# Performance work log

Measured on AMD Instinct MI355X. Metric: run time of the kernel, lower is better.

## Reference

```python
import jax, jax.numpy as jnp
import numpy as np

B, S, V, E, H, L = 16, 256, 32000, 512, 1024, 2


def setup_inputs() -> dict:
    key = jax.random.key(0)
    ks = jax.random.split(key, 10)
    scale = 0.02
    tokens = jax.random.randint(ks[0], (B, S), 1, V)  # avoid pad token 0
    emb = jax.random.normal(ks[1], (V, E), dtype=jnp.float32) * scale
    W0 = jax.random.normal(ks[2], (E, 4 * H), dtype=jnp.float32) * scale
    U0 = jax.random.normal(ks[3], (H, 4 * H), dtype=jnp.float32) * scale
    b0 = jnp.zeros((4 * H,), dtype=jnp.float32)
    W1 = jax.random.normal(ks[4], (H, 4 * H), dtype=jnp.float32) * scale
    U1 = jax.random.normal(ks[5], (H, 4 * H), dtype=jnp.float32) * scale
    b1 = jnp.zeros((4 * H,), dtype=jnp.float32)
    Wd = jax.random.normal(ks[6], (H, V), dtype=jnp.float32) * scale
    bd = jnp.zeros((V,), dtype=jnp.float32)
    return {"tokens": tokens, "emb": emb, "W0": W0, "U0": U0, "b0": b0,
            "W1": W1, "U1": U1, "b1": b1, "Wd": Wd, "bd": bd}


def lstm_layer(x, mask, W, U, b):
    """Keras LSTM (gate order i,f,g,o), mask carries state/output on padded steps.
    x: [B,S,D], mask: [B,S] bool -> (ys [B,S,H], h [B,H], c [B,H])."""
    h_dim = U.shape[0]
    bsz = x.shape[0]
    x_t = jnp.swapaxes(x, 0, 1)           # [S,B,D]
    m_t = jnp.swapaxes(mask, 0, 1)        # [S,B]

    def step(carry, inp):
        h, c = carry
        xt, mt = inp
        z = xt @ W + h @ U + b            # [B,4H]
        i, f, g, o = jnp.split(z, 4, axis=-1)
        c_new = jax.nn.sigmoid(f) * c + jax.nn.sigmoid(i) * jnp.tanh(g)
        h_new = jax.nn.sigmoid(o) * jnp.tanh(c_new)
        mt = mt[:, None]
        h_new = jnp.where(mt, h_new, h)
        c_new = jnp.where(mt, c_new, c)
        return (h_new, c_new), h_new

    init = (jnp.zeros((bsz, h_dim), x.dtype), jnp.zeros((bsz, h_dim), x.dtype))
    (h, c), ys = jax.lax.scan(step, init, (x_t, m_t))
    return jnp.swapaxes(ys, 0, 1), h, c


def reference(tokens, emb, W0, U0, b0, W1, U1, b1, Wd, bd):
    mask = tokens != 0                    # mask_zero=True in Embedding
    x = emb[tokens]                       # [B,S,E]
    x, h0, c0 = lstm_layer(x, mask, W0, U0, b0)
    x, h1, c1 = lstm_layer(x, mask, W1, U1, b1)
    probs = jax.nn.softmax(x @ Wd + bd, axis=-1)  # Dense(softmax) -> [B,S,V]
    h_stack = jnp.stack([h0, h1])         # [L,B,H] final hidden states
    c_stack = jnp.stack([c0, c1])         # [L,B,H] final cell states
    return probs, h_stack, c_stack
```

## Files before the change

kernel.cpp:

```cpp
#include <hip/hip_runtime.h>

typedef __attribute__((ext_vector_type(8))) short bf16x8;
typedef __attribute__((ext_vector_type(4))) float f32x4;

#define S_LEN 256
#define VOCAB 32000
#define EMB   512
#define HID   1024

static const size_t OUT_H = 131072000ull;

__device__ inline unsigned short f2bf(float f) {
  unsigned int u = __float_as_uint(f);
  u = (u + 0x7FFFu + ((u >> 16) & 1u)) >> 16;
  return (unsigned short)u;
}
__device__ inline float bf2f(unsigned short s) {
  return __uint_as_float(((unsigned int)s) << 16);
}

__device__ inline void st_h(unsigned short* p, unsigned short v) {
  __hip_atomic_store(p, v, __ATOMIC_RELAXED, __HIP_MEMORY_SCOPE_AGENT);
}

__device__ inline int xcd_swz(int o, int n) {
  int q = n >> 3, r = n & 7;
  int x = o & 7, i = o >> 3;
  return (x < r ? x * (q + 1) : r * (q + 1) + (x - r) * q) + i;
}

__device__ inline void gload16(const void* g, void* lds) {
  __builtin_amdgcn_global_load_lds((const __attribute__((address_space(1))) unsigned int*)g,
                                   (__attribute__((address_space(3))) unsigned int*)lds,
                                   16, 0, 0);
}

__global__ __launch_bounds__(256) void k_transpose_bf16(const float* __restrict__ src,
                                                        unsigned short* __restrict__ dst,
                                                        int K, int N) {
  __shared__ float tile[64][65];
  int n0 = blockIdx.x * 64, k0 = blockIdx.y * 64;
  int tid = threadIdx.x;
#pragma unroll
  for (int i = 0; i < 16; ++i) {
    int e = tid + i * 256;
    int r = e >> 6, c = e & 63;
    tile[r][c] = src[(size_t)(k0 + r) * N + n0 + c];
  }
  __syncthreads();
#pragma unroll
  for (int i = 0; i < 16; ++i) {
    int e = tid + i * 256;
    int r = e >> 6, c = e & 63;
    dst[(size_t)(n0 + r) * K + k0 + c] = f2bf(tile[c][r]);
  }
}

__global__ __launch_bounds__(256) void k_gather_emb(const int* __restrict__ tokens,
                                                    const float* __restrict__ emb,
                                                    unsigned short* __restrict__ Xg) {
  int r = blockIdx.x;
  int s = r >> 4, b = r & 15;
  int tok = tokens[b * S_LEN + s];
  const float* src = emb + (size_t)tok * EMB;
  int k = threadIdx.x * 2;
  float2 v = *(const float2*)(src + k);
  ushort2 o; o.x = f2bf(v.x); o.y = f2bf(v.y);
  *(ushort2*)(Xg + (size_t)r * EMB + k) = o;
}

__global__ __launch_bounds__(256) void k_gemm128(const unsigned short* __restrict__ A,
                                                 const unsigned short* __restrict__ BT,
                                                 float* __restrict__ C,
                                                 const float* __restrict__ bias,
                                                 int M, int N, int K) {
  __shared__ unsigned short As[4096];
  __shared__ unsigned short Bs[4096];
  int tid = threadIdx.x;
  int lane = tid & 63, wv = tid >> 6;
  int wr = wv >> 1, wc = wv & 1;
  int bxs = xcd_swz(blockIdx.x, gridDim.x);
  int am0 = blockIdx.y * 128, bn0 = bxs * 128;
  f32x4 zero = {0.f, 0.f, 0.f, 0.f};
  f32x4 acc[4][4];
#pragma unroll
  for (int m = 0; m < 4; ++m)
#pragma unroll
    for (int n = 0; n < 4; ++n) acc[m][n] = zero;
  int KT = K >> 5;
  int lr = lane & 15, kq = lane >> 4;
  for (int kt = 0; kt < KT; ++kt) {
    int k0 = kt << 5;
    __syncthreads();
#pragma unroll
    for (int c = 0; c < 2; ++c) {
      int t2 = c * 256 + tid;
      int row = t2 & 127, kg = t2 >> 7;
      gload16(A + (size_t)(am0 + row) * K + k0 + kg * 8, &As[(c * 256 + wv * 64) * 8]);
    }
#pragma unroll
    for (int c = 0; c < 2; ++c) {
      int t2 = c * 256 + tid;
      int row = t2 & 127, kg = t2 >> 7;
      gload16(BT + (size_t)(bn0 + row) * K + k0 + kg * 8, &Bs[(c * 256 + wv * 64) * 8]);
    }
    __syncthreads();
    const bf16x8* Ap = (const bf16x8*)As;
    const bf16x8* Bp = (const bf16x8*)Bs;
    bf16x8 af[4], bf[4];
#pragma unroll
    for (int m = 0; m < 4; ++m) af[m] = Ap[kq * 128 + wr * 64 + m * 16 + lr];
#pragma unroll
    for (int n = 0; n < 4; ++n) bf[n] = Bp[kq * 128 + wc * 64 + n * 16 + lr];
#pragma unroll
    for (int m = 0; m < 4; ++m)
#pragma unroll
      for (int n = 0; n < 4; ++n)
        acc[m][n] = __builtin_amdgcn_mfma_f32_16x16x32_bf16(af[m], bf[n], acc[m][n], 0, 0, 0);
  }
#pragma unroll
  for (int m = 0; m < 4; ++m)
#pragma unroll
    for (int n = 0; n < 4; ++n) {
      int col = bn0 + wc * 64 + n * 16 + lr;
      float bv = bias ? bias[col] : 0.f;
#pragma unroll
      for (int q = 0; q < 4; ++q) {
        int row = am0 + wr * 64 + m * 16 + kq * 4 + q;
        C[(size_t)row * N + col] = acc[m][n][q] + bv;
      }
    }
}

__global__ __launch_bounds__(512, 2) void k_gemm256(const unsigned short* __restrict__ A,
                                                    const unsigned short* __restrict__ BT,
                                                    unsigned short* __restrict__ Cb,
                                                    const float* __restrict__ bias,
                                                    int M, int N, int K,
                                                    float* __restrict__ Mpart,
                                                    float* __restrict__ Spart,
                                                    int NT) {
  extern __shared__ unsigned short lds[];
  int tid = threadIdx.x;
  int w = tid >> 6, lane = tid & 63;
  int wr = w >> 2, wcn = w & 3;
  int lr = lane & 15, kq = lane >> 4, sw = lr & 7;
  int bxs = xcd_swz(blockIdx.x, gridDim.x);
  int gm0 = blockIdx.y * 256, gn0 = bxs * 256;
  const int KT = K >> 6;

  f32x4 acc[8][4];
#pragma unroll
  for (int m = 0; m < 8; ++m)
#pragma unroll
    for (int n = 0; n < 4; ++n) acc[m][n] = f32x4{0.f, 0.f, 0.f, 0.f};

  auto stage = [&](const unsigned short* g, int grow0, int kt, int mat, int half) {
    unsigned short* sb = lds + ((((kt & 1) * 2 + mat) * 2 + half) << 13);
#pragma unroll
    for (int ld = 0; ld < 2; ++ld) {
      int j = ld * 512 + tid;
      int row = j >> 3, c16 = j & 7;
      const unsigned short* src =
          g + (size_t)(grow0 + half * 128 + row) * K + kt * 64 + ((c16 ^ (row & 7)) << 3);
      gload16(src, sb + ((ld * 512 + w * 64) << 3));
    }
  };

  stage(A, gm0, 0, 0, 0); stage(A, gm0, 0, 0, 1);
  stage(BT, gn0, 0, 1, 0); stage(BT, gn0, 0, 1, 1);
  stage(BT, gn0, 1, 1, 0); stage(BT, gn0, 1, 1, 1);
  asm volatile("s_waitcnt vmcnt(4)" ::: "memory");
  __builtin_amdgcn_sched_barrier(0);
  __builtin_amdgcn_s_barrier();

  const int halfB = wcn >> 1;
  const int rowB0 = (wcn & 1) * 64;

  for (int i = 0; i < KT / 2; ++i) {
    int kt0 = 2 * i, kt1 = 2 * i + 1;
#pragma unroll
    for (int half = 0; half < 2; ++half) {
      int kt = half ? kt1 : kt0;
      int buf = kt & 1;
      const unsigned short* ldsA = lds + (((buf * 2 + 0) * 2 + wr) << 13);
      const unsigned short* ldsB = lds + (((buf * 2 + 1) * 2 + halfB) << 13);
      bf16x8 bf[4][2];
#pragma unroll
      for (int qd = 0; qd < 4; ++qd) {
        if (qd == 0) {
#pragma unroll
          for (int fn = 0; fn < 4; ++fn)
#pragma unroll
            for (int kk = 0; kk < 2; ++kk) {
              int r = rowB0 + fn * 16 + lr;
              int c = (kk * 4 + kq) ^ sw;
              bf[fn][kk] = *(const bf16x8*)(ldsB + r * 64 + c * 8);
            }
        }
        bf16x8 af[2][2];
#pragma unroll
        for (int m2 = 0; m2 < 2; ++m2)
#pragma unroll
          for (int kk = 0; kk < 2; ++kk) {
            int r = (qd * 2 + m2) * 16 + lr;
            int c = (kk * 4 + kq) ^ sw;
            af[m2][kk] = *(const bf16x8*)(ldsA + r * 64 + c * 8);
          }
        if (half == 0) {
          if (qd == 0) { stage(A, gm0, kt0 + 1, 0, 0); stage(A, gm0, kt0 + 1, 0, 1); }
          else if (qd == 1) { if (kt0 + 2 < KT) stage(BT, gn0, kt0 + 2, 1, 0); }
          else if (qd == 2) { if (kt0 + 2 < KT) stage(BT, gn0, kt0 + 2, 1, 1); }
          else {
            if (kt0 + 2 < KT) asm volatile("s_waitcnt vmcnt(4)" ::: "memory");
            else              asm volatile("s_waitcnt vmcnt(0)" ::: "memory");
          }
        } else {
          if (qd == 0)      { if (kt1 + 1 < KT) stage(A, gm0, kt1 + 1, 0, 0); }
          else if (qd == 1) { if (kt1 + 1 < KT) stage(A, gm0, kt1 + 1, 0, 1); }
          else if (qd == 2) { if (kt1 + 2 < KT) stage(BT, gn0, kt1 + 2, 1, 0); }
          else {
            if (kt1 + 2 < KT) { stage(BT, gn0, kt1 + 2, 1, 1);
                                asm volatile("s_waitcnt vmcnt(4)" ::: "memory"); }
            else              asm volatile("s_waitcnt vmcnt(0)" ::: "memory");
          }
        }
        __builtin_amdgcn_sched_barrier(0);
        __builtin_amdgcn_s_barrier();
        asm volatile("s_waitcnt lgkmcnt(0)" ::: "memory");
        __builtin_amdgcn_sched_barrier(0);
        __builtin_amdgcn_s_setprio(1);
#pragma unroll
        for (int m2 = 0; m2 < 2; ++m2)
#pragma unroll
          for (int n = 0; n < 4; ++n)
#pragma unroll
            for (int kk = 0; kk < 2; ++kk)
              acc[qd * 2 + m2][n] =
                  __builtin_amdgcn_mfma_f32_16x16x32_bf16(af[m2][kk], bf[n][kk],
                                                          acc[qd * 2 + m2][n], 0, 0, 0);
        __builtin_amdgcn_s_setprio(0);
        __builtin_amdgcn_sched_barrier(0);
        __builtin_amdgcn_s_barrier();
      }
    }
  }

  asm volatile("s_waitcnt vmcnt(0) lgkmcnt(0)" ::: "memory");
  __syncthreads();

  float bvc[4];
#pragma unroll
  for (int n = 0; n < 4; ++n) bvc[n] = bias[gn0 + wcn * 64 + n * 16 + lr];
#pragma unroll
  for (int fm = 0; fm < 8; ++fm)
#pragma unroll
    for (int n = 0; n < 4; ++n) {
      int col = gn0 + wcn * 64 + n * 16 + lr;
#pragma unroll
      for (int q = 0; q < 4; ++q) {
        int row = gm0 + wr * 128 + fm * 16 + kq * 4 + q;
        Cb[(size_t)row * N + col] = f2bf(acc[fm][n][q] + bvc[n]);
      }
    }
  float* redM = (float*)lds;
  float* redS = (float*)lds + 1024;
#pragma unroll
  for (int fm = 0; fm < 8; ++fm)
#pragma unroll
    for (int q = 0; q < 4; ++q) {
      float mx = fmaxf(fmaxf(acc[fm][0][q] + bvc[0], acc[fm][1][q] + bvc[1]),
                       fmaxf(acc[fm][2][q] + bvc[2], acc[fm][3][q] + bvc[3]));
#pragma unroll
      for (int off = 1; off < 16; off <<= 1) mx = fmaxf(mx, __shfl_xor(mx, off));
      if (lr == 0) redM[(wr * 4 + wcn) * 128 + fm * 16 + kq * 4 + q] = mx;
    }
  __syncthreads();
#pragma unroll
  for (int fm = 0; fm < 8; ++fm)
#pragma unroll
    for (int q = 0; q < 4; ++q) {
      int idx = fm * 16 + kq * 4 + q;
      float mxF = fmaxf(fmaxf(redM[(wr * 4 + 0) * 128 + idx], redM[(wr * 4 + 1) * 128 + idx]),
                        fmaxf(redM[(wr * 4 + 2) * 128 + idx], redM[(wr * 4 + 3) * 128 + idx]));
      float s = __expf(acc[fm][0][q] + bvc[0] - mxF) + __expf(acc[fm][1][q] + bvc[1] - mxF) +
                __expf(acc[fm][2][q] + bvc[2] - mxF) + __expf(acc[fm][3][q] + bvc[3] - mxF);
#pragma unroll
      for (int off = 1; off < 16; off <<= 1) s += __shfl_xor(s, off);
      if (lr == 0) redS[(wr * 4 + wcn) * 128 + idx] = s;
    }
  __syncthreads();
  if (wcn == 0 && lr == 0) {
#pragma unroll
    for (int fm = 0; fm < 8; ++fm)
#pragma unroll
      for (int q = 0; q < 4; ++q) {
        int idx = fm * 16 + kq * 4 + q;
        float mxF = fmaxf(fmaxf(redM[(wr * 4 + 0) * 128 + idx], redM[(wr * 4 + 1) * 128 + idx]),
                          fmaxf(redM[(wr * 4 + 2) * 128 + idx], redM[(wr * 4 + 3) * 128 + idx]));
        float ss = redS[(wr * 4 + 0) * 128 + idx] + redS[(wr * 4 + 1) * 128 + idx] +
                   redS[(wr * 4 + 2) * 128 + idx] + redS[(wr * 4 + 3) * 128 + idx];
        int row = gm0 + wr * 128 + idx;
        Mpart[(size_t)row * NT + bxs] = mxF;
        Spart[(size_t)row * NT + bxs] = ss;
      }
  }
}

__global__ __launch_bounds__(256) void k_sm_combine(const float* __restrict__ Mp,
                                                    const float* __restrict__ Sp,
                                                    float* __restrict__ MS, int T) {
  int row = blockIdx.x * 4 + (threadIdx.x >> 6);
  int lane = threadIdx.x & 63;
  float mx = -3.4e38f;
  for (int i = lane; i < T; i += 64) mx = fmaxf(mx, Mp[(size_t)row * T + i]);
#pragma unroll
  for (int o = 32; o > 0; o >>= 1) mx = fmaxf(mx, __shfl_xor(mx, o));
  float s = 0.f;
  for (int i = lane; i < T; i += 64)
    s += Sp[(size_t)row * T + i] * __expf(Mp[(size_t)row * T + i] - mx);
#pragma unroll
  for (int o = 32; o > 0; o >>= 1) s += __shfl_xor(s, o);
  if (lane == 0) { MS[row * 2] = mx; MS[row * 2 + 1] = 1.f / s; }
}

__global__ __launch_bounds__(256) void k_sm_apply_bf16(const unsigned short* __restrict__ lg,
                                                       float* __restrict__ probs,
                                                       const float* __restrict__ MS) {
  const int total = 4096 * (VOCAB / 4);
  for (int idx = blockIdx.x * 256 + threadIdx.x; idx < total; idx += gridDim.x * 256) {
    int row = idx / (VOCAB / 4);
    float M = MS[row * 2], inv = MS[row * 2 + 1];
    ushort4 v = ((const ushort4*)lg)[idx];
    float4 o;
    o.x = __expf(bf2f(v.x) - M) * inv;
    o.y = __expf(bf2f(v.y) - M) * inv;
    o.z = __expf(bf2f(v.z) - M) * inv;
    o.w = __expf(bf2f(v.w) - M) * inv;
    ((float4*)probs)[idx] = o;
  }
}

struct LstmSmem {
  unsigned short U0s[16384];
  unsigned short W1s[16384];
  unsigned short U1s[16384];
  float zA[4][16][16];
  float zB[4][16][16];
  float c0[16][4], h0f[16][4], c1[16][4], h1f[16][4];
  float b1s[16];
  short toks[16][256];
  unsigned short h0st[16][4], h1st[16][4];
};

__global__ __launch_bounds__(256, 1) void k_lstm(const int* __restrict__ tokens,
                                                 const float* __restrict__ XW,
                                                 const unsigned short* __restrict__ U0T,
                                                 const unsigned short* __restrict__ W1T,
                                                 const unsigned short* __restrict__ U1T,
                                                 const float* __restrict__ b1,
                                                 unsigned short* __restrict__ h0r,
                                                 unsigned short* __restrict__ h1r,
                                                 unsigned short* __restrict__ Y1,
                                                 float* outHC,
                                                 int* bar) {
  extern __shared__ char smraw[];
  LstmSmem& sm = *(LstmSmem*)smraw;
  int tid = threadIdx.x, bid = blockIdx.x;
  int lane = tid & 63, wv = tid >> 6;

  for (int idx = tid; idx < 2048; idx += 256) {
    int cidx = idx >> 7, kg = idx & 127;
    int gcol = (cidx >> 2) * 1024 + bid * 4 + (cidx & 3);
    *(uint4*)&sm.U0s[(kg * 16 + cidx) * 8] = *(const uint4*)&U0T[(size_t)gcol * 1024 + kg * 8];
    *(uint4*)&sm.W1s[(kg * 16 + cidx) * 8] = *(const uint4*)&W1T[(size_t)gcol * 1024 + kg * 8];
    *(uint4*)&sm.U1s[(kg * 16 + cidx) * 8] = *(const uint4*)&U1T[(size_t)gcol * 1024 + kg * 8];
  }
  for (int idx = tid; idx < 4096; idx += 256) {
    sm.toks[idx >> 8][idx & 255] = (short)tokens[idx];
  }
  if (tid < 64) {
    int b = tid >> 2, u = tid & 3;
    sm.c0[b][u] = 0.f; sm.h0f[b][u] = 0.f;
    sm.c1[b][u] = 0.f; sm.h1f[b][u] = 0.f;
  }
  if (tid < 16) sm.b1s[tid] = b1[(tid >> 2) * 1024 + bid * 4 + (tid & 3)];
  __syncthreads();

  int lr = lane & 15, kq = lane >> 4;

  auto gbar = [&](int gen) {
    __syncthreads();
    if (tid == 0)
      __hip_atomic_store(&bar[bid * 16], gen, __ATOMIC_RELAXED, __HIP_MEMORY_SCOPE_AGENT);
    int ok;
    do {
      int f = __hip_atomic_load(&bar[tid * 16], __ATOMIC_RELAXED, __HIP_MEMORY_SCOPE_AGENT);
      ok = (f >= gen);
    } while (!__syncthreads_and(ok));
  };

  if (wv == 1) {
    int l = tid - 64, b = l >> 2, u = l & 3;
    const float* xp = XW + (size_t)b * 4096 + bid * 4 + u;
    float z0 = xp[0], z2 = xp[2048], z3 = xp[3072];
    float ii = 1.f / (1.f + expf(-z0));
    float gg = tanhf(z2);
    float oo = 1.f / (1.f + expf(-z3));
    float cn = ii * gg;
    float hn = oo * tanhf(cn);
    if (sm.toks[b][0] == 0) { cn = 0.f; hn = 0.f; }
    sm.c0[b][u] = cn; sm.h0f[b][u] = hn;
    st_h(h0r + b * HID + bid * 4 + u, f2bf(hn));
  }
  gbar(1);

  for (int t = 0; t < 255; ++t) {
    const unsigned short* h0t = h0r + (size_t)t * 16384;
    const unsigned short* h1p = h1r + (size_t)(t > 0 ? t - 1 : 0) * 16384;
    unsigned short* h1c = h1r + (size_t)t * 16384;
    unsigned short* h0n = h0r + (size_t)(t + 1) * 16384;

    float xwv0 = 0, xwv1 = 0, xwv2 = 0, xwv3 = 0;
    if (wv == 1) {
      int l = tid - 64, b = l >> 2, u = l & 3;
      const float* xp = XW + ((size_t)(t + 1) * 16 + b) * 4096 + bid * 4 + u;
      xwv0 = xp[0]; xwv1 = xp[1024]; xwv2 = xp[2048]; xwv3 = xp[3072];
    }

    f32x4 accB = {0.f, 0.f, 0.f, 0.f};
    {
      const unsigned short* ap = (wv < 2) ? h0t : h1p;
      const unsigned short* bm = (wv < 2) ? sm.W1s : sm.U1s;
      int kofs = (wv & 1) * 512;
      if (wv < 2 || t > 0) {
#pragma unroll
        for (int s8 = 0; s8 < 16; ++s8) {
          int kb = kofs + s8 * 32;
          bf16x8 av = *(const bf16x8*)(ap + lr * HID + kb + kq * 8);
          bf16x8 bv = *(const bf16x8*)&bm[(((kb >> 3) + kq) * 16 + lr) * 8];
          accB = __builtin_amdgcn_mfma_f32_16x16x32_bf16(av, bv, accB, 0, 0, 0);
        }
      }
    }
    f32x4 accA = {0.f, 0.f, 0.f, 0.f};
#pragma unroll
    for (int s8 = 0; s8 < 8; ++s8) {
      int kb = wv * 256 + s8 * 32;
      bf16x8 av = *(const bf16x8*)(h0t + lr * HID + kb + kq * 8);
      bf16x8 bv = *(const bf16x8*)&sm.U0s[(((kb >> 3) + kq) * 16 + lr) * 8];
      accA = __builtin_amdgcn_mfma_f32_16x16x32_bf16(av, bv, accA, 0, 0, 0);
    }
#pragma unroll
    for (int q = 0; q < 4; ++q) {
      sm.zB[wv][kq * 4 + q][lr] = accB[q];
      sm.zA[wv][kq * 4 + q][lr] = accA[q];
    }
    __syncthreads();

    if (wv == 0) {
      int b = tid >> 2, u = tid & 3;
      int tok = sm.toks[b][t];
      float z0 = sm.b1s[0 + u]  + sm.zB[0][b][0 + u]  + sm.zB[1][b][0 + u]  + sm.zB[2][b][0 + u]  + sm.zB[3][b][0 + u];
      float z1 = sm.b1s[4 + u]  + sm.zB[0][b][4 + u]  + sm.zB[1][b][4 + u]  + sm.zB[2][b][4 + u]  + sm.zB[3][b][4 + u];
      float z2 = sm.b1s[8 + u]  + sm.zB[0][b][8 + u]  + sm.zB[1][b][8 + u]  + sm.zB[2][b][8 + u]  + sm.zB[3][b][8 + u];
      float z3 = sm.b1s[12 + u] + sm.zB[0][b][12 + u] + sm.zB[1][b][12 + u] + sm.zB[2][b][12 + u] + sm.zB[3][b][12 + u];
      float ii = 1.f / (1.f + expf(-z0));
      float ff = 1.f / (1.f + expf(-z1));
      float gg = tanhf(z2);
      float oo = 1.f / (1.f + expf(-z3));
      float cold = sm.c1[b][u], hold = sm.h1f[b][u];
      float cn = ff * cold + ii * gg;
      float hn = oo * tanhf(cn);
      if (tok == 0) { cn = cold; hn = hold; }
      sm.c1[b][u] = cn; sm.h1f[b][u] = hn;
      unsigned short hb = f2bf(hn);
      sm.h1st[b][u] = hb;
      Y1[((size_t)b * S_LEN + t) * HID + bid * 4 + u] = hb;
    } else if (wv == 1) {
      int l = tid - 64, b = l >> 2, u = l & 3;
      int tok = sm.toks[b][t + 1];
      float z0 = xwv0 + sm.zA[0][b][0 + u]  + sm.zA[1][b][0 + u]  + sm.zA[2][b][0 + u]  + sm.zA[3][b][0 + u];
      float z1 = xwv1 + sm.zA[0][b][4 + u]  + sm.zA[1][b][4 + u]  + sm.zA[2][b][4 + u]  + sm.zA[3][b][4 + u];
      float z2 = xwv2 + sm.zA[0][b][8 + u]  + sm.zA[1][b][8 + u]  + sm.zA[2][b][8 + u]  + sm.zA[3][b][8 + u];
      float z3 = xwv3 + sm.zA[0][b][12 + u] + sm.zA[1][b][12 + u] + sm.zA[2][b][12 + u] + sm.zA[3][b][12 + u];
      float ii = 1.f / (1.f + expf(-z0));
      float ff = 1.f / (1.f + expf(-z1));
      float gg = tanhf(z2);
      float oo = 1.f / (1.f + expf(-z3));
      float cold = sm.c0[b][u], hold = sm.h0f[b][u];
      float cn = ff * cold + ii * gg;
      float hn = oo * tanhf(cn);
      if (tok == 0) { cn = cold; hn = hold; }
      sm.c0[b][u] = cn; sm.h0f[b][u] = hn;
      sm.h0st[b][u] = f2bf(hn);
    }
    __syncthreads();
    if (tid < 32) {
      int b = tid & 15;
      unsigned long long v = *(const unsigned long long*)((tid < 16) ? &sm.h1st[b][0]
                                                                     : &sm.h0st[b][0]);
      unsigned short* dst = (tid < 16) ? (h1c + b * HID + bid * 4)
                                       : (h0n + b * HID + bid * 4);
      __hip_atomic_store((unsigned long long*)dst, v, __ATOMIC_RELAXED,
                         __HIP_MEMORY_SCOPE_AGENT);
    }
    gbar(t + 2);
  }

  {
    const unsigned short* h0t = h0r + 255ull * 16384;
    const unsigned short* h1p = h1r + 254ull * 16384;
    f32x4 accB = {0.f, 0.f, 0.f, 0.f};
    const unsigned short* ap = (wv < 2) ? h0t : h1p;
    const unsigned short* bm = (wv < 2) ? sm.W1s : sm.U1s;
    int kofs = (wv & 1) * 512;
#pragma unroll
    for (int s8 = 0; s8 < 16; ++s8) {
      int kb = kofs + s8 * 32;
      bf16x8 av = *(const bf16x8*)(ap + lr * HID + kb + kq * 8);
      bf16x8 bv = *(const bf16x8*)&bm[(((kb >> 3) + kq) * 16 + lr) * 8];
      accB = __builtin_amdgcn_mfma_f32_16x16x32_bf16(av, bv, accB, 0, 0, 0);
    }
#pragma unroll
    for (int q = 0; q < 4; ++q) sm.zB[wv][kq * 4 + q][lr] = accB[q];
    __syncthreads();
    if (wv == 0) {
      int b = tid >> 2, u = tid & 3;
      int tok = sm.toks[b][255];
      float z0 = sm.b1s[0 + u]  + sm.zB[0][b][0 + u]  + sm.zB[1][b][0 + u]  + sm.zB[2][b][0 + u]  + sm.zB[3][b][0 + u];
      float z1 = sm.b1s[4 + u]  + sm.zB[0][b][4 + u]  + sm.zB[1][b][4 + u]  + sm.zB[2][b][4 + u]  + sm.zB[3][b][4 + u];
      float z2 = sm.b1s[8 + u]  + sm.zB[0][b][8 + u]  + sm.zB[1][b][8 + u]  + sm.zB[2][b][8 + u]  + sm.zB[3][b][8 + u];
      float z3 = sm.b1s[12 + u] + sm.zB[0][b][12 + u] + sm.zB[1][b][12 + u] + sm.zB[2][b][12 + u] + sm.zB[3][b][12 + u];
      float ii = 1.f / (1.f + expf(-z0));
      float ff = 1.f / (1.f + expf(-z1));
      float gg = tanhf(z2);
      float oo = 1.f / (1.f + expf(-z3));
      float cold = sm.c1[b][u], hold = sm.h1f[b][u];
      float cn = ff * cold + ii * gg;
      float hn = oo * tanhf(cn);
      if (tok == 0) { cn = cold; hn = hold; }
      sm.c1[b][u] = cn; sm.h1f[b][u] = hn;
      Y1[((size_t)b * S_LEN + 255) * HID + bid * 4 + u] = f2bf(hn);
    }
    __syncthreads();
  }

  if (tid < 64) {
    int b = tid >> 2, u = tid & 3, ug = bid * 4 + u;
    outHC[OUT_H + (size_t)b * HID + ug]         = sm.h0f[b][u];
    outHC[OUT_H + 16384 + (size_t)b * HID + ug] = sm.h1f[b][u];
    outHC[OUT_H + 32768 + (size_t)b * HID + ug] = sm.c0[b][u];
    outHC[OUT_H + 49152 + (size_t)b * HID + ug] = sm.c1[b][u];
  }
}

extern "C" void kernel_launch(void* const* d_in, const int* in_sizes, int n_in,
                              void* d_out, int out_size, void* d_ws, size_t ws_size,
                              hipStream_t stream) {
  const int*   tokens = (const int*)d_in[0];
  const float* emb = (const float*)d_in[1];
  const float* W0  = (const float*)d_in[2];
  const float* U0  = (const float*)d_in[3];
  const float* b0  = (const float*)d_in[4];
  const float* W1  = (const float*)d_in[5];
  const float* U1  = (const float*)d_in[6];
  const float* b1  = (const float*)d_in[7];
  const float* Wd  = (const float*)d_in[8];
  const float* bd  = (const float*)d_in[9];
  float* out = (float*)d_out;

  char* ws = (char*)d_ws;
  size_t off = 0;
  auto alloc = [&](size_t bytes) { char* p = ws + off; off += (bytes + 255) & ~(size_t)255; return p; };
  unsigned short* W0T = (unsigned short*)alloc(4096ull * 512 * 2);
  unsigned short* U0T = (unsigned short*)alloc(4096ull * 1024 * 2);
  unsigned short* W1T = (unsigned short*)alloc(4096ull * 1024 * 2);
  unsigned short* U1T = (unsigned short*)alloc(4096ull * 1024 * 2);
  unsigned short* WdT = (unsigned short*)alloc(32000ull * 1024 * 2);
  unsigned short* Xg  = (unsigned short*)alloc(4096ull * 512 * 2);
  unsigned short* Y1  = (unsigned short*)alloc(4096ull * 1024 * 2);
  int*   bar   = (int*)alloc(16384);
  float* Mpart = (float*)alloc(4096ull * 125 * 4);
  float* Spart = (float*)alloc(4096ull * 125 * 4);
  float* MS    = (float*)alloc(4096ull * 2 * 4);
  unsigned short* Lb = (unsigned short*)alloc(4096ull * VOCAB * 2);

  float* XW = out;
  unsigned short* h0r = (unsigned short*)((char*)d_out + 192ull * 1024 * 1024);
  unsigned short* h1r = (unsigned short*)((char*)d_out + 208ull * 1024 * 1024);

  hipMemsetAsync(bar, 0, 16384, stream);

  hipFuncSetAttribute((const void*)k_lstm, hipFuncAttributeMaxDynamicSharedMemorySize,
                      (int)sizeof(LstmSmem));
  hipFuncSetAttribute((const void*)k_gemm256, hipFuncAttributeMaxDynamicSharedMemorySize,
                      131072);

  k_transpose_bf16<<<dim3(64, 8), 256, 0, stream>>>(W0, W0T, 512, 4096);
  k_transpose_bf16<<<dim3(64, 16), 256, 0, stream>>>(U0, U0T, 1024, 4096);
  k_transpose_bf16<<<dim3(64, 16), 256, 0, stream>>>(W1, W1T, 1024, 4096);
  k_transpose_bf16<<<dim3(64, 16), 256, 0, stream>>>(U1, U1T, 1024, 4096);
  k_transpose_bf16<<<dim3(500, 16), 256, 0, stream>>>(Wd, WdT, 1024, 32000);
  k_gather_emb<<<4096, 256, 0, stream>>>(tokens, emb, Xg);

  k_gemm128<<<dim3(32, 32), 256, 0, stream>>>(Xg, W0T, XW, b0, 4096, 4096, 512);

  k_lstm<<<256, 256, sizeof(LstmSmem), stream>>>(tokens, XW, U0T, W1T, U1T, b1,
                                                 h0r, h1r, Y1, out, bar);

  k_gemm256<<<dim3(125, 16), 512, 131072, stream>>>(Y1, WdT, Lb, bd, 4096, 32000, 1024,
                                                    Mpart, Spart, 125);
  k_sm_combine<<<1024, 256, 0, stream>>>(Mpart, Spart, MS, 125);
  k_sm_apply_bf16<<<4096, 256, 0, stream>>>(Lb, out, MS);
}
```

Baseline: 2.150 ms.

## Drop Y1 buffer, feed LSTM ring output to dense GEMM with row remap

The LSTM no longer writes a separate batch-major Y1 output. The final dense GEMM instead reads the time-major h1 ring buffer directly and remaps output rows back to batch-major order. The input-projection GEMM is switched from the 128-tile kernel to a templated 256-tile kernel with fp32 output, and three weight transposes are merged into one launch. This removes scattered per-step global stores from the latency-bound recurrence and some launch overhead, at the cost of scattered rows in the dense GEMM's epilogue writes.

```diff
diff --git a/kernel.cpp b/kernel.cpp
--- a/kernel.cpp
+++ b/kernel.cpp
@@ -39,6 +39,33 @@
                                                         unsigned short* __restrict__ dst,
                                                         int K, int N) {
   __shared__ float tile[64][65];
+  int n0 = blockIdx.x * 64, k0 = blockIdx.y * 64;
+  int tid = threadIdx.x;
+#pragma unroll
+  for (int i = 0; i < 16; ++i) {
+    int e = tid + i * 256;
+    int r = e >> 6, c = e & 63;
+    tile[r][c] = src[(size_t)(k0 + r) * N + n0 + c];
+  }
+  __syncthreads();
+#pragma unroll
+  for (int i = 0; i < 16; ++i) {
+    int e = tid + i * 256;
+    int r = e >> 6, c = e & 63;
+    dst[(size_t)(n0 + r) * K + k0 + c] = f2bf(tile[c][r]);
+  }
+}
+
+__global__ __launch_bounds__(256) void k_transpose3(const float* __restrict__ s0,
+                                                    const float* __restrict__ s1,
+                                                    const float* __restrict__ s2,
+                                                    unsigned short* __restrict__ d0,
+                                                    unsigned short* __restrict__ d1,
+                                                    unsigned short* __restrict__ d2) {
+  __shared__ float tile[64][65];
+  const float* src = (blockIdx.z == 0) ? s0 : (blockIdx.z == 1) ? s1 : s2;
+  unsigned short* dst = (blockIdx.z == 0) ? d0 : (blockIdx.z == 1) ? d1 : d2;
+  const int K = 1024, N = 4096;
   int n0 = blockIdx.x * 64, k0 = blockIdx.y * 64;
   int tid = threadIdx.x;
 #pragma unroll
@@ -69,71 +96,10 @@
   *(ushort2*)(Xg + (size_t)r * EMB + k) = o;
 }
 
-__global__ __launch_bounds__(256) void k_gemm128(const unsigned short* __restrict__ A,
-                                                 const unsigned short* __restrict__ BT,
-                                                 float* __restrict__ C,
-                                                 const float* __restrict__ bias,
-                                                 int M, int N, int K) {
-  __shared__ unsigned short As[4096];
-  __shared__ unsigned short Bs[4096];
-  int tid = threadIdx.x;
-  int lane = tid & 63, wv = tid >> 6;
-  int wr = wv >> 1, wc = wv & 1;
-  int bxs = xcd_swz(blockIdx.x, gridDim.x);
-  int am0 = blockIdx.y * 128, bn0 = bxs * 128;
-  f32x4 zero = {0.f, 0.f, 0.f, 0.f};
-  f32x4 acc[4][4];
-#pragma unroll
-  for (int m = 0; m < 4; ++m)
-#pragma unroll
-    for (int n = 0; n < 4; ++n) acc[m][n] = zero;
-  int KT = K >> 5;
-  int lr = lane & 15, kq = lane >> 4;
-  for (int kt = 0; kt < KT; ++kt) {
-    int k0 = kt << 5;
-    __syncthreads();
-#pragma unroll
-    for (int c = 0; c < 2; ++c) {
-      int t2 = c * 256 + tid;
-      int row = t2 & 127, kg = t2 >> 7;
-      gload16(A + (size_t)(am0 + row) * K + k0 + kg * 8, &As[(c * 256 + wv * 64) * 8]);
-    }
-#pragma unroll
-    for (int c = 0; c < 2; ++c) {
-      int t2 = c * 256 + tid;
-      int row = t2 & 127, kg = t2 >> 7;
-      gload16(BT + (size_t)(bn0 + row) * K + k0 + kg * 8, &Bs[(c * 256 + wv * 64) * 8]);
-    }
-    __syncthreads();
-    const bf16x8* Ap = (const bf16x8*)As;
-    const bf16x8* Bp = (const bf16x8*)Bs;
-    bf16x8 af[4], bf[4];
-#pragma unroll
-    for (int m = 0; m < 4; ++m) af[m] = Ap[kq * 128 + wr * 64 + m * 16 + lr];
-#pragma unroll
-    for (int n = 0; n < 4; ++n) bf[n] = Bp[kq * 128 + wc * 64 + n * 16 + lr];
-#pragma unroll
-    for (int m = 0; m < 4; ++m)
-#pragma unroll
-      for (int n = 0; n < 4; ++n)
-        acc[m][n] = __builtin_amdgcn_mfma_f32_16x16x32_bf16(af[m], bf[n], acc[m][n], 0, 0, 0);
-  }
-#pragma unroll
-  for (int m = 0; m < 4; ++m)
-#pragma unroll
-    for (int n = 0; n < 4; ++n) {
-      int col = bn0 + wc * 64 + n * 16 + lr;
-      float bv = bias ? bias[col] : 0.f;
-#pragma unroll
-      for (int q = 0; q < 4; ++q) {
-        int row = am0 + wr * 64 + m * 16 + kq * 4 + q;
-        C[(size_t)row * N + col] = acc[m][n][q] + bv;
-      }
-    }
-}
-
+template <bool BF16OUT, bool SMPART, bool REMAP>
 __global__ __launch_bounds__(512, 2) void k_gemm256(const unsigned short* __restrict__ A,
                                                     const unsigned short* __restrict__ BT,
+                                                    float* __restrict__ Cf,
                                                     unsigned short* __restrict__ Cb,
                                                     const float* __restrict__ bias,
                                                     int M, int N, int K,
@@ -259,38 +225,28 @@
       int col = gn0 + wcn * 64 + n * 16 + lr;
 #pragma unroll
       for (int q = 0; q < 4; ++q) {
-        int row = gm0 + wr * 128 + fm * 16 + kq * 4 + q;
-        Cb[(size_t)row * N + col] = f2bf(acc[fm][n][q] + bvc[n]);
+        int r = gm0 + wr * 128 + fm * 16 + kq * 4 + q;
+        int row = REMAP ? (((r & 15) << 8) | (r >> 4)) : r;
+        if constexpr (BF16OUT)
+          Cb[(size_t)row * N + col] = f2bf(acc[fm][n][q] + bvc[n]);
+        else
+          Cf[(size_t)row * N + col] = acc[fm][n][q] + bvc[n];
       }
     }
-  float* redM = (float*)lds;
-  float* redS = (float*)lds + 1024;
-#pragma unroll
-  for (int fm = 0; fm < 8; ++fm)
-#pragma unroll
-    for (int q = 0; q < 4; ++q) {
-      float mx = fmaxf(fmaxf(acc[fm][0][q] + bvc[0], acc[fm][1][q] + bvc[1]),
-                       fmaxf(acc[fm][2][q] + bvc[2], acc[fm][3][q] + bvc[3]));
-#pragma unroll
-      for (int off = 1; off < 16; off <<= 1) mx = fmaxf(mx, __shfl_xor(mx, off));
-      if (lr == 0) redM[(wr * 4 + wcn) * 128 + fm * 16 + kq * 4 + q] = mx;
-    }
-  __syncthreads();
-#pragma unroll
-  for (int fm = 0; fm < 8; ++fm)
-#pragma unroll
-    for (int q = 0; q < 4; ++q) {
-      int idx = fm * 16 + kq * 4 + q;
-      float mxF = fmaxf(fmaxf(redM[(wr * 4 + 0) * 128 + idx], redM[(wr * 4 + 1) * 128 + idx]),
-                        fmaxf(redM[(wr * 4 + 2) * 128 + idx], redM[(wr * 4 + 3) * 128 + idx]));
-      float s = __expf(acc[fm][0][q] + bvc[0] - mxF) + __expf(acc[fm][1][q] + bvc[1] - mxF) +
-                __expf(acc[fm][2][q] + bvc[2] - mxF) + __expf(acc[fm][3][q] + bvc[3] - mxF);
-#pragma unroll
-      for (int off = 1; off < 16; off <<= 1) s += __shfl_xor(s, off);
-      if (lr == 0) redS[(wr * 4 + wcn) * 128 + idx] = s;
-    }
-  __syncthreads();
-  if (wcn == 0 && lr == 0) {
+  if constexpr (SMPART) {
+    float* redM = (float*)lds;
+    float* redS = (float*)lds + 1024;
+#pragma unroll
+    for (int fm = 0; fm < 8; ++fm)
+#pragma unroll
+      for (int q = 0; q < 4; ++q) {
+        float mx = fmaxf(fmaxf(acc[fm][0][q] + bvc[0], acc[fm][1][q] + bvc[1]),
+                         fmaxf(acc[fm][2][q] + bvc[2], acc[fm][3][q] + bvc[3]));
+#pragma unroll
+        for (int off = 1; off < 16; off <<= 1) mx = fmaxf(mx, __shfl_xor(mx, off));
+        if (lr == 0) redM[(wr * 4 + wcn) * 128 + fm * 16 + kq * 4 + q] = mx;
+      }
+    __syncthreads();
 #pragma unroll
     for (int fm = 0; fm < 8; ++fm)
 #pragma unroll
@@ -298,12 +254,29 @@
         int idx = fm * 16 + kq * 4 + q;
         float mxF = fmaxf(fmaxf(redM[(wr * 4 + 0) * 128 + idx], redM[(wr * 4 + 1) * 128 + idx]),
                           fmaxf(redM[(wr * 4 + 2) * 128 + idx], redM[(wr * 4 + 3) * 128 + idx]));
-        float ss = redS[(wr * 4 + 0) * 128 + idx] + redS[(wr * 4 + 1) * 128 + idx] +
-                   redS[(wr * 4 + 2) * 128 + idx] + redS[(wr * 4 + 3) * 128 + idx];
-        int row = gm0 + wr * 128 + idx;
-        Mpart[(size_t)row * NT + bxs] = mxF;
-        Spart[(size_t)row * NT + bxs] = ss;
+        float s = __expf(acc[fm][0][q] + bvc[0] - mxF) + __expf(acc[fm][1][q] + bvc[1] - mxF) +
+                  __expf(acc[fm][2][q] + bvc[2] - mxF) + __expf(acc[fm][3][q] + bvc[3] - mxF);
+#pragma unroll
+        for (int off = 1; off < 16; off <<= 1) s += __shfl_xor(s, off);
+        if (lr == 0) redS[(wr * 4 + wcn) * 128 + idx] = s;
       }
+    __syncthreads();
+    if (wcn == 0 && lr == 0) {
+#pragma unroll
+      for (int fm = 0; fm < 8; ++fm)
+#pragma unroll
+        for (int q = 0; q < 4; ++q) {
+          int idx = fm * 16 + kq * 4 + q;
+          float mxF = fmaxf(fmaxf(redM[(wr * 4 + 0) * 128 + idx], redM[(wr * 4 + 1) * 128 + idx]),
+                            fmaxf(redM[(wr * 4 + 2) * 128 + idx], redM[(wr * 4 + 3) * 128 + idx]));
+          float ss = redS[(wr * 4 + 0) * 128 + idx] + redS[(wr * 4 + 1) * 128 + idx] +
+                     redS[(wr * 4 + 2) * 128 + idx] + redS[(wr * 4 + 3) * 128 + idx];
+          int r = gm0 + wr * 128 + idx;
+          int row = REMAP ? (((r & 15) << 8) | (r >> 4)) : r;
+          Mpart[(size_t)row * NT + bxs] = mxF;
+          Spart[(size_t)row * NT + bxs] = ss;
+        }
+    }
   }
 }
 
@@ -361,7 +334,6 @@
                                                  const float* __restrict__ b1,
                                                  unsigned short* __restrict__ h0r,
                                                  unsigned short* __restrict__ h1r,
-                                                 unsigned short* __restrict__ Y1,
                                                  float* outHC,
                                                  int* bar) {
   extern __shared__ char smraw[];
@@ -474,9 +446,7 @@
       float hn = oo * tanhf(cn);
       if (tok == 0) { cn = cold; hn = hold; }
       sm.c1[b][u] = cn; sm.h1f[b][u] = hn;
-      unsigned short hb = f2bf(hn);
-      sm.h1st[b][u] = hb;
-      Y1[((size_t)b * S_LEN + t) * HID + bid * 4 + u] = hb;
+      sm.h1st[b][u] = f2bf(hn);
     } else if (wv == 1) {
       int l = tid - 64, b = l >> 2, u = l & 3;
       int tok = sm.toks[b][t + 1];
@@ -541,7 +511,7 @@
       float hn = oo * tanhf(cn);
       if (tok == 0) { cn = cold; hn = hold; }
       sm.c1[b][u] = cn; sm.h1f[b][u] = hn;
-      Y1[((size_t)b * S_LEN + 255) * HID + bid * 4 + u] = f2bf(hn);
+      h1r[255ull * 16384 + b * HID + bid * 4 + u] = f2bf(hn);
     }
     __syncthreads();
   }
@@ -579,7 +549,6 @@
   unsigned short* U1T = (unsigned short*)alloc(4096ull * 1024 * 2);
   unsigned short* WdT = (unsigned short*)alloc(32000ull * 1024 * 2);
   unsigned short* Xg  = (unsigned short*)alloc(4096ull * 512 * 2);
-  unsigned short* Y1  = (unsigned short*)alloc(4096ull * 1024 * 2);
   int*   bar   = (int*)alloc(16384);
   float* Mpart = (float*)alloc(4096ull * 125 * 4);
   float* Spart = (float*)alloc(4096ull * 125 * 4);
@@ -594,23 +563,24 @@
 
   hipFuncSetAttribute((const void*)k_lstm, hipFuncAttributeMaxDynamicSharedMemorySize,
                       (int)sizeof(LstmSmem));
-  hipFuncSetAttribute((const void*)k_gemm256, hipFuncAttributeMaxDynamicSharedMemorySize,
-                      131072);
+  hipFuncSetAttribute((const void*)k_gemm256<false, false, false>,
+                      hipFuncAttributeMaxDynamicSharedMemorySize, 131072);
+  hipFuncSetAttribute((const void*)k_gemm256<true, true, true>,
+                      hipFuncAttributeMaxDynamicSharedMemorySize, 131072);
 
   k_transpose_bf16<<<dim3(64, 8), 256, 0, stream>>>(W0, W0T, 512, 4096);
-  k_transpose_bf16<<<dim3(64, 16), 256, 0, stream>>>(U0, U0T, 1024, 4096);
-  k_transpose_bf16<<<dim3(64, 16), 256, 0, stream>>>(W1, W1T, 1024, 4096);
-  k_transpose_bf16<<<dim3(64, 16), 256, 0, stream>>>(U1, U1T, 1024, 4096);
+  k_transpose3<<<dim3(64, 16, 3), 256, 0, stream>>>(U0, W1, U1, U0T, W1T, U1T);
   k_transpose_bf16<<<dim3(500, 16), 256, 0, stream>>>(Wd, WdT, 1024, 32000);
   k_gather_emb<<<4096, 256, 0, stream>>>(tokens, emb, Xg);
 
-  k_gemm128<<<dim3(32, 32), 256, 0, stream>>>(Xg, W0T, XW, b0, 4096, 4096, 512);
+  k_gemm256<false, false, false><<<dim3(16, 16), 512, 131072, stream>>>(
+      Xg, W0T, XW, nullptr, b0, 4096, 4096, 512, nullptr, nullptr, 0);
 
   k_lstm<<<256, 256, sizeof(LstmSmem), stream>>>(tokens, XW, U0T, W1T, U1T, b1,
-                                                 h0r, h1r, Y1, out, bar);
-
-  k_gemm256<<<dim3(125, 16), 512, 131072, stream>>>(Y1, WdT, Lb, bd, 4096, 32000, 1024,
-                                                    Mpart, Spart, 125);
+                                                 h0r, h1r, out, bar);
+
+  k_gemm256<true, true, true><<<dim3(125, 16), 512, 131072, stream>>>(
+      h1r, WdT, nullptr, Lb, bd, 4096, 32000, 1024, Mpart, Spart, 125);
   k_sm_combine<<<1024, 256, 0, stream>>>(Mpart, Spart, MS, 125);
   k_sm_apply_bf16<<<4096, 256, 0, stream>>>(Lb, out, MS);
 }
```

After: 2.109 ms. No clear change (-1.9%).
